# Kernel optimization log

Measured on AMD Instinct MI355X. Metric: run time of the kernel, lower is better.

The kernel has to match this reference:

```python
import jax, jax.numpy as jnp
import numpy as np

V, C, T, E, H, L = 25, 8, 14, 64, 128, 32
B = 65536


def setup_inputs() -> dict:
    key = jax.random.key(0)
    ks = jax.random.split(key, 24)
    rn = lambda k, s: jax.random.normal(k, s, dtype=jnp.float32) * 0.05
    return {
        "x": jax.random.randint(ks[0], (B, T), 0, V),
        "c": jax.random.normal(ks[1], (B, C), dtype=jnp.float32),
        "eps": jax.random.normal(ks[2], (B, L), dtype=jnp.float32),
        # encoder params
        "emb_enc": rn(ks[3], (V, E)),
        "W_ih_e": rn(ks[4], (3 * H, E)),
        "W_hh_e": rn(ks[5], (3 * H, H)),
        "b_ih_e": rn(ks[6], (3 * H,)),
        "b_hh_e": rn(ks[7], (3 * H,)),
        "W_mu": rn(ks[8], (L, H + C)),
        "b_mu": rn(ks[9], (L,)),
        "W_lv": rn(ks[10], (L, H + C)),
        "b_lv": rn(ks[11], (L,)),
        # decoder params
        "emb_dec": rn(ks[12], (V, E)),
        "W_fch": rn(ks[13], (H, L + C)),
        "b_fch": rn(ks[14], (H,)),
        "W_ih_d": rn(ks[15], (3 * H, E + L + C)),
        "W_hh_d": rn(ks[16], (3 * H, H)),
        "b_ih_d": rn(ks[17], (3 * H,)),
        "b_hh_d": rn(ks[18], (3 * H,)),
        "W_out": rn(ks[19], (V, H)),
        "b_out": rn(ks[20], (V,)),
    }


def gru_seq(x_proj, h0, W_hh, b_hh):
    """PyTorch-style GRU. x_proj: [B,T,3H] = input @ W_ih.T + b_ih (precomputed)."""
    def step(h, xp):
        gh = h @ W_hh.T + b_hh
        i_r, i_z, i_n = jnp.split(xp, 3, axis=-1)
        h_r, h_z, h_n = jnp.split(gh, 3, axis=-1)
        r = jax.nn.sigmoid(i_r + h_r)
        zg = jax.nn.sigmoid(i_z + h_z)
        n = jnp.tanh(i_n + r * h_n)
        h_new = (1.0 - zg) * n + zg * h
        return h_new, h_new
    hT, hs = jax.lax.scan(step, h0, jnp.swapaxes(x_proj, 0, 1))
    return hT, hs  # hs: [T,B,H]


def reference(x, c, eps, emb_enc, W_ih_e, W_hh_e, b_ih_e, b_hh_e, W_mu, b_mu,
              W_lv, b_lv, emb_dec, W_fch, b_fch, W_ih_d, W_hh_d, b_ih_d,
              b_hh_d, W_out, b_out):
    Bn = x.shape[0]
    Hn = W_hh_e.shape[1]
    # ---- encoder ----
    emb = emb_enc[x]                                   # [B,T,E]
    xp = emb @ W_ih_e.T + b_ih_e                       # [B,T,3H]
    h_enc, _ = gru_seq(xp, jnp.zeros((Bn, Hn), emb.dtype), W_hh_e, b_hh_e)
    hc = jnp.concatenate([h_enc, c], axis=1)           # [B,H+C]
    mu = hc @ W_mu.T + b_mu
    logvar = hc @ W_lv.T + b_lv
    # ---- reparameterize ----
    z = mu + eps * jnp.exp(0.5 * logvar)
    # ---- decoder (teacher forced on x[:, :-1]) ----
    context = jnp.concatenate([z, c], axis=1)          # [B,L+C]
    h0 = context @ W_fch.T + b_fch                     # [B,H]
    dec_in = x[:, :-1]                                 # [B,T-1]
    emb_d = emb_dec[dec_in]                            # [B,T-1,E]
    Tm1 = dec_in.shape[1]
    ctx_b = jnp.broadcast_to(context[:, None, :], (Bn, Tm1, context.shape[1]))
    step_in = jnp.concatenate([emb_d, ctx_b], axis=-1)  # [B,T-1,E+L+C]
    xp_d = step_in @ W_ih_d.T + b_ih_d                 # [B,T-1,3H]
    _, hs = gru_seq(xp_d, h0, W_hh_d, b_hh_d)          # [T-1,B,H]
    recon = jnp.einsum('tbh,vh->btv', hs, W_out) + b_out  # [B,T-1,V]
    return recon, mu, logvar
```

## Files before the change

### kernel.cpp

```cpp
#include <hip/hip_runtime.h>

typedef __bf16 bf16x8 __attribute__((ext_vector_type(8)));
typedef __bf16 bf16x4 __attribute__((ext_vector_type(4)));
typedef float  floatx4 __attribute__((ext_vector_type(4)));

#define Vv 25
#define Tt 14
#define Ee 64
#define Hh 128
#define Ll 32
#define Ccc 8
#define G3 384
#define TABP 388
#define HP   136
#define CXP  72

#define MFMA16(a, b, c) __builtin_amdgcn_mfma_f32_16x16x32_bf16(a, b, c, 0, 0, 0)

extern "C" __global__ void __launch_bounds__(256)
cvae_tables(const float* __restrict__ emb_enc, const float* __restrict__ W_ih_e,
            const float* __restrict__ b_ih_e, const float* __restrict__ b_hh_e,
            const float* __restrict__ emb_dec, const float* __restrict__ W_ih_d,
            float* __restrict__ ws)
{
    int id = blockIdx.x * 256 + threadIdx.x;
    if (id >= 2 * Vv * G3) return;
    int half = id / (Vv * G3);
    int r = id % (Vv * G3);
    int v = r / G3, j = r % G3;
    if (half == 0) {
        float acc = b_ih_e[j] + (j < 2 * Hh ? b_hh_e[j] : 0.0f);
        const float* e = emb_enc + v * Ee;
        const float* wp = W_ih_e + j * Ee;
        #pragma unroll 4
        for (int k = 0; k < Ee; k++) acc += e[k] * wp[k];
        ws[v * G3 + j] = acc;
    } else {
        float acc = 0.0f;
        const float* e = emb_dec + v * Ee;
        const float* wp = W_ih_d + j * 104;
        #pragma unroll 4
        for (int k = 0; k < Ee; k++) acc += e[k] * wp[k];
        ws[Vv * G3 + v * G3 + j] = acc;
    }
}

__device__ __forceinline__ float rcp_f(float x) { return __builtin_amdgcn_rcpf(x); }
__device__ __forceinline__ float sigm(float x)  { return rcp_f(1.0f + __expf(-x)); }
__device__ __forceinline__ float tanhg(float x) { return 1.0f - 2.0f * rcp_f(1.0f + __expf(2.0f * x)); }

extern "C" __global__ void __launch_bounds__(512, 2)
cvae_mfma(const int* __restrict__ x, const float* __restrict__ cin,
          const float* __restrict__ eps,
          const float* __restrict__ W_hh_e, const float* __restrict__ b_hh_e,
          const float* __restrict__ W_mu, const float* __restrict__ b_mu,
          const float* __restrict__ W_lv, const float* __restrict__ b_lv,
          const float* __restrict__ W_fch, const float* __restrict__ b_fch,
          const float* __restrict__ W_ih_d, const float* __restrict__ W_hh_d,
          const float* __restrict__ b_ih_d, const float* __restrict__ b_hh_d,
          const float* __restrict__ W_out, const float* __restrict__ b_out,
          const float* __restrict__ tabs, float* __restrict__ out, int Btot)
{
    __shared__ __align__(16) __bf16 hA[64 * HP];
    __shared__ __align__(16) __bf16 hB[64 * HP];
    __shared__ __align__(16) __bf16 tab_s[Vv * TABP];
    __shared__ __align__(16) __bf16 ctx_s[64 * CXP];
    __shared__ unsigned char x_s[64 * Tt];

    const int tid  = threadIdx.x;
    const int w    = tid >> 6;
    const int lane = tid & 63;
    const int li   = lane & 15;
    const int q    = lane >> 4;
    const int b0   = blockIdx.x * 64;
    const size_t MU_OFF = (size_t)Btot * 13 * Vv;
    const size_t LV_OFF = MU_OFF + (size_t)Btot * Ll;
    const floatx4 zf = {0.f, 0.f, 0.f, 0.f};

    for (int i = tid; i < 64 * Tt; i += 512)
        x_s[i] = (unsigned char)x[(size_t)b0 * Tt + i];
    for (int i = tid; i < Vv * G3; i += 512)
        tab_s[(i / G3) * TABP + (i % G3)] = (__bf16)tabs[i];
    {
        int b = tid >> 3, cc = tid & 7;
        ctx_s[b * CXP + Ll + cc] = (__bf16)cin[((size_t)b0 + b) * Ccc + cc];
        #pragma unroll
        for (int k3 = 0; k3 < 3; k3++) {
            int i = tid * 3 + k3;
            ctx_s[(i / 24) * CXP + 40 + (i % 24)] = (__bf16)0.f;
        }
    }

    bf16x8 aW[3][4];
    #pragma unroll
    for (int role = 0; role < 3; role++)
        #pragma unroll
        for (int kb = 0; kb < 4; kb++) {
            const float* p = W_hh_e + (role * Hh + w * 16 + li) * Hh + kb * 32 + q * 8;
            bf16x8 f;
            #pragma unroll
            for (int jj = 0; jj < 8; jj++) f[jj] = (__bf16)p[jj];
            aW[role][kb] = f;
        }
    float bhh2[4];
    #pragma unroll
    for (int r = 0; r < 4; r++) bhh2[r] = b_hh_e[2 * Hh + w * 16 + q * 4 + r];

    float hreg[4][4];
    #pragma unroll
    for (int nt = 0; nt < 4; nt++)
        #pragma unroll
        for (int r = 0; r < 4; r++) hreg[nt][r] = 0.f;

    __syncthreads();

    for (int t = 0; t < Tt; t++) {
        const __bf16* rd = (t & 1) ? hB : hA;
        __bf16*       wr = (t & 1) ? hA : hB;

        floatx4 acc[3][4];
        if (t == 0) {
            #pragma unroll
            for (int role = 0; role < 3; role++)
                #pragma unroll
                for (int nt = 0; nt < 4; nt++) acc[role][nt] = zf;
        } else {
            bf16x8 hf[4][4];
            #pragma unroll
            for (int nt = 0; nt < 4; nt++)
                #pragma unroll
                for (int kb = 0; kb < 4; kb++)
                    hf[nt][kb] = *(const bf16x8*)&rd[(nt * 16 + li) * HP + kb * 32 + q * 8];
            #pragma unroll
            for (int role = 0; role < 3; role++)
                #pragma unroll
                for (int nt = 0; nt < 4; nt++) acc[role][nt] = zf;
            #pragma unroll
            for (int kb = 0; kb < 4; kb++)
                #pragma unroll
                for (int role = 0; role < 3; role++)
                    #pragma unroll
                    for (int nt = 0; nt < 4; nt++)
                        acc[role][nt] = MFMA16(aW[role][kb], hf[nt][kb], acc[role][nt]);
        }

        #pragma unroll
        for (int nt = 0; nt < 4; nt++) {
            int bl = nt * 16 + li;
            int tok = x_s[bl * Tt + t];
            const __bf16* tp = &tab_s[tok * TABP + w * 16 + q * 4];
            bf16x4 tR = *(const bf16x4*)(tp);
            bf16x4 tZ = *(const bf16x4*)(tp + Hh);
            bf16x4 tN = *(const bf16x4*)(tp + 2 * Hh);
            bf16x4 hv;
            #pragma unroll
            for (int r = 0; r < 4; r++) {
                float rr = sigm(acc[0][nt][r] + (float)tR[r]);
                float zz = sigm(acc[1][nt][r] + (float)tZ[r]);
                float nn = tanhg((float)tN[r] + rr * (acc[2][nt][r] + bhh2[r]));
                float h  = nn + zz * (hreg[nt][r] - nn);
                hreg[nt][r] = h;
                hv[r] = (__bf16)h;
            }
            *(bf16x4*)&wr[bl * HP + w * 16 + q * 4] = hv;
        }
        __syncthreads();
    }

    {
        for (int i = tid; i < Vv * G3; i += 512)
            tab_s[(i / G3) * TABP + (i % G3)] = (__bf16)tabs[Vv * G3 + i];

        const int mt = w & 3;
        const int lp = mt * 8 + (li >> 1);
        const float* Wsrc = (li & 1) ? W_lv : W_mu;
        bf16x8 aM[5], aE[5];
        #pragma unroll
        for (int kb = 0; kb < 5; kb++) {
            bf16x8 f = {}, f2 = {};
            if (kb < 4 || q == 0) {
                const float* p = Wsrc + lp * 136 + (kb < 4 ? kb * 32 + q * 8 : 128);
                #pragma unroll
                for (int jj = 0; jj < 8; jj++) {
                    float v = p[jj];
                    __bf16 hi = (__bf16)v;
                    f[jj]  = hi;
                    f2[jj] = (__bf16)(v - (float)hi);
                }
            }
            aM[kb] = f; aE[kb] = f2;
        }
        #pragma unroll
        for (int jn = 0; jn < 2; jn++) {
            const int nt = (w >> 2) * 2 + jn;
            floatx4 acc = zf;
            #pragma unroll
            for (int kb = 0; kb < 4; kb++) {
                bf16x8 hf = *(const bf16x8*)&hA[(nt * 16 + li) * HP + kb * 32 + q * 8];
                acc = MFMA16(aM[kb], hf, acc);
                acc = MFMA16(aE[kb], hf, acc);
            }
            {
                bf16x8 cf = {};
                if (q == 0) cf = *(const bf16x8*)&ctx_s[(nt * 16 + li) * CXP + Ll];
                acc = MFMA16(aM[4], cf, acc);
                acc = MFMA16(aE[4], cf, acc);
            }
            const int b = nt * 16 + li;
            const size_t bg = (size_t)b0 + b;
            const int l0 = mt * 8 + q * 2;
            float mu0 = acc[0] + b_mu[l0],     lv0 = acc[1] + b_lv[l0];
            float mu1 = acc[2] + b_mu[l0 + 1], lv1 = acc[3] + b_lv[l0 + 1];
            float2 ev = *(const float2*)&eps[bg * Ll + l0];
            float z0 = mu0 + ev.x * __expf(0.5f * lv0);
            float z1 = mu1 + ev.y * __expf(0.5f * lv1);
            ctx_s[b * CXP + l0]     = (__bf16)z0;
            ctx_s[b * CXP + l0 + 1] = (__bf16)z1;
            *(float2*)&out[MU_OFF + bg * Ll + l0] = make_float2(mu0, mu1);
            *(float2*)&out[LV_OFF + bg * Ll + l0] = make_float2(lv0, lv1);
        }
    }
    __syncthreads();

    floatx4 h0a[4] = {zf, zf, zf, zf};
    floatx4 base[3][4];
    #pragma unroll
    for (int role = 0; role < 3; role++)
        #pragma unroll
        for (int nt = 0; nt < 4; nt++) base[role][nt] = zf;
    #pragma unroll
    for (int kb2 = 0; kb2 < 2; kb2++) {
        bf16x8 afh, aC0, aC1, aC2;
        #pragma unroll
        for (int jj = 0; jj < 8; jj++) {
            int k = kb2 * 32 + q * 8 + jj;
            bool ok = (k < 40);
            afh[jj] = ok ? (__bf16)W_fch[(w * 16 + li) * 40 + k]                   : (__bf16)0.f;
            aC0[jj] = ok ? (__bf16)W_ih_d[(0 * Hh + w * 16 + li) * 104 + Ee + k]   : (__bf16)0.f;
            aC1[jj] = ok ? (__bf16)W_ih_d[(1 * Hh + w * 16 + li) * 104 + Ee + k]   : (__bf16)0.f;
            aC2[jj] = ok ? (__bf16)W_ih_d[(2 * Hh + w * 16 + li) * 104 + Ee + k]   : (__bf16)0.f;
        }
        #pragma unroll
        for (int nt = 0; nt < 4; nt++) {
            bf16x8 cf = *(const bf16x8*)&ctx_s[(nt * 16 + li) * CXP + kb2 * 32 + q * 8];
            h0a[nt]     = MFMA16(afh, cf, h0a[nt]);
            base[0][nt] = MFMA16(aC0, cf, base[0][nt]);
            base[1][nt] = MFMA16(aC1, cf, base[1][nt]);
            base[2][nt] = MFMA16(aC2, cf, base[2][nt]);
        }
    }
    #pragma unroll
    for (int nt = 0; nt < 4; nt++) {
        bf16x4 hv;
        #pragma unroll
        for (int r = 0; r < 4; r++) {
            float s = h0a[nt][r] + b_fch[w * 16 + q * 4 + r];
            hreg[nt][r] = s;
            hv[r] = (__bf16)s;
        }
        *(bf16x4*)&hA[(nt * 16 + li) * HP + w * 16 + q * 4] = hv;
    }
    float bhn[4];
    #pragma unroll
    for (int r = 0; r < 4; r++) {
        int j = w * 16 + q * 4 + r;
        float br = b_ih_d[j] + b_hh_d[j];
        float bz = b_ih_d[Hh + j] + b_hh_d[Hh + j];
        float bi = b_ih_d[2 * Hh + j];
        #pragma unroll
        for (int nt = 0; nt < 4; nt++) {
            base[0][nt][r] += br;
            base[1][nt][r] += bz;
            base[2][nt][r] += bi;
        }
        bhn[r] = b_hh_d[2 * Hh + j];
    }
    #pragma unroll
    for (int role = 0; role < 3; role++)
        #pragma unroll
        for (int kb = 0; kb < 4; kb++) {
            const float* p = W_hh_d + (role * Hh + w * 16 + li) * Hh + kb * 32 + q * 8;
            bf16x8 f;
            #pragma unroll
            for (int jj = 0; jj < 8; jj++) f[jj] = (__bf16)p[jj];
            aW[role][kb] = f;
        }
    const int mt_o = w & 1, nt_o = w >> 1;
    bf16x8 aO[4];
    #pragma unroll
    for (int kb = 0; kb < 4; kb++) {
        int row = mt_o * 16 + li;
        bf16x8 f;
        #pragma unroll
        for (int jj = 0; jj < 8; jj++)
            f[jj] = (row < Vv) ? (__bf16)W_out[row * Hh + kb * 32 + q * 8 + jj] : (__bf16)0.f;
        aO[kb] = f;
    }
    float bo[4];
    #pragma unroll
    for (int r = 0; r < 4; r++) {
        int v = mt_o * 16 + q * 4 + r;
        bo[r] = (v < Vv) ? b_out[v] : 0.f;
    }

    __syncthreads();

    for (int t = 0; t < Tt - 1; t++) {
        const __bf16* rdb = (t & 1) ? hB : hA;
        __bf16*       wrb = (t & 1) ? hA : hB;

        bf16x8 hf[4][4];
        #pragma unroll
        for (int nt = 0; nt < 4; nt++)
            #pragma unroll
            for (int kb = 0; kb < 4; kb++)
                hf[nt][kb] = *(const bf16x8*)&rdb[(nt * 16 + li) * HP + kb * 32 + q * 8];

        floatx4 acc[3][4];
        #pragma unroll
        for (int nt = 0; nt < 4; nt++) {
            acc[0][nt] = base[0][nt];
            acc[1][nt] = base[1][nt];
            acc[2][nt] = zf;
        }
        #pragma unroll
        for (int kb = 0; kb < 4; kb++)
            #pragma unroll
            for (int role = 0; role < 3; role++)
                #pragma unroll
                for (int nt = 0; nt < 4; nt++)
                    acc[role][nt] = MFMA16(aW[role][kb], hf[nt][kb], acc[role][nt]);

        #pragma unroll
        for (int nt = 0; nt < 4; nt++) {
            int bl = nt * 16 + li;
            int tok = x_s[bl * Tt + t];
            const __bf16* tp = &tab_s[tok * TABP + w * 16 + q * 4];
            bf16x4 tR = *(const bf16x4*)(tp);
            bf16x4 tZ = *(const bf16x4*)(tp + Hh);
            bf16x4 tN = *(const bf16x4*)(tp + 2 * Hh);
            bf16x4 hv;
            #pragma unroll
            for (int r = 0; r < 4; r++) {
                float rr = sigm(acc[0][nt][r] + (float)tR[r]);
                float zz = sigm(acc[1][nt][r] + (float)tZ[r]);
                float nn = tanhg(base[2][nt][r] + (float)tN[r] + rr * (acc[2][nt][r] + bhn[r]));
                float h  = nn + zz * (hreg[nt][r] - nn);
                hreg[nt][r] = h;
                hv[r] = (__bf16)h;
            }
            *(bf16x4*)&wrb[bl * HP + w * 16 + q * 4] = hv;
        }
        __syncthreads();

        bf16x8 of[4];
        #pragma unroll
        for (int kb = 0; kb < 4; kb++)
            of[kb] = *(const bf16x8*)&wrb[(nt_o * 16 + li) * HP + kb * 32 + q * 8];
        floatx4 po = zf;
        #pragma unroll
        for (int kb = 0; kb < 4; kb++)
            po = MFMA16(aO[kb], of[kb], po);
        #pragma unroll
        for (int r = 0; r < 4; r++) {
            int v = mt_o * 16 + q * 4 + r;
            if (v < Vv)
                out[((size_t)(b0 + nt_o * 16 + li) * 13 + t) * Vv + v] = po[r] + bo[r];
        }
    }
}

extern "C" void kernel_launch(void* const* d_in, const int* in_sizes, int n_in,
                              void* d_out, int out_size, void* d_ws, size_t ws_size,
                              hipStream_t stream)
{
    const int*   x       = (const int*)d_in[0];
    const float* c       = (const float*)d_in[1];
    const float* eps     = (const float*)d_in[2];
    const float* emb_enc = (const float*)d_in[3];
    const float* W_ih_e  = (const float*)d_in[4];
    const float* W_hh_e  = (const float*)d_in[5];
    const float* b_ih_e  = (const float*)d_in[6];
    const float* b_hh_e  = (const float*)d_in[7];
    const float* W_mu    = (const float*)d_in[8];
    const float* b_mu    = (const float*)d_in[9];
    const float* W_lv    = (const float*)d_in[10];
    const float* b_lv    = (const float*)d_in[11];
    const float* emb_dec = (const float*)d_in[12];
    const float* W_fch   = (const float*)d_in[13];
    const float* b_fch   = (const float*)d_in[14];
    const float* W_ih_d  = (const float*)d_in[15];
    const float* W_hh_d  = (const float*)d_in[16];
    const float* b_ih_d  = (const float*)d_in[17];
    const float* b_hh_d  = (const float*)d_in[18];
    const float* W_out   = (const float*)d_in[19];
    const float* b_out   = (const float*)d_in[20];

    float* ws = (float*)d_ws;
    const int Btot = in_sizes[0] / Tt;

    cvae_tables<<<75, 256, 0, stream>>>(emb_enc, W_ih_e, b_ih_e, b_hh_e, emb_dec, W_ih_d, ws);

    cvae_mfma<<<Btot / 64, 512, 0, stream>>>(
        x, c, eps, W_hh_e, b_hh_e, W_mu, b_mu, W_lv, b_lv,
        W_fch, b_fch, W_ih_d, W_hh_d, b_ih_d, b_hh_d, W_out, b_out,
        ws, (float*)d_out, Btot);
}
```

Measured before the change: 568.2 us.

## Replace LDS token table gathers with one-hot MFMA and raise occupancy

Drops the shared-memory copy of the per-token input projection tables and computes each gate's input contribution with an extra MFMA per gate, multiplying a register-resident slice of the table by a one-hot vector built from the token id. This removes roughly 19 KB of LDS and the scattered bf16x4 table reads on each step, and launch bounds are raised from 2 to 4 blocks per SM. The cost is 12 extra MFMAs per step, register pressure from holding the table slices, and a risk of spilling under the tighter register cap.

```diff
diff --git a/kernel.cpp b/kernel.cpp
--- a/kernel.cpp
+++ b/kernel.cpp
@@ -3,6 +3,7 @@
 typedef __bf16 bf16x8 __attribute__((ext_vector_type(8)));
 typedef __bf16 bf16x4 __attribute__((ext_vector_type(4)));
 typedef float  floatx4 __attribute__((ext_vector_type(4)));
+typedef unsigned int u32x4 __attribute__((ext_vector_type(4)));
 
 #define Vv 25
 #define Tt 14
@@ -11,7 +12,6 @@
 #define Ll 32
 #define Ccc 8
 #define G3 384
-#define TABP 388
 #define HP   136
 #define CXP  72
 
@@ -49,7 +49,20 @@
 __device__ __forceinline__ float sigm(float x)  { return rcp_f(1.0f + __expf(-x)); }
 __device__ __forceinline__ float tanhg(float x) { return 1.0f - 2.0f * rcp_f(1.0f + __expf(2.0f * x)); }
 
-extern "C" __global__ void __launch_bounds__(512, 2)
+__device__ __forceinline__ bf16x8 onehot8(int tok, int q)
+{
+    int u = tok - q * 8;
+    unsigned val = (u & 1) ? 0x3F800000u : 0x00003F80u;
+    int uw = u >> 1;
+    u32x4 wds;
+    wds[0] = (uw == 0) ? val : 0u;
+    wds[1] = (uw == 1) ? val : 0u;
+    wds[2] = (uw == 2) ? val : 0u;
+    wds[3] = (uw == 3) ? val : 0u;
+    return __builtin_bit_cast(bf16x8, wds);
+}
+
+extern "C" __global__ void __launch_bounds__(512, 4)
 cvae_mfma(const int* __restrict__ x, const float* __restrict__ cin,
           const float* __restrict__ eps,
           const float* __restrict__ W_hh_e, const float* __restrict__ b_hh_e,
@@ -63,7 +76,6 @@
 {
     __shared__ __align__(16) __bf16 hA[64 * HP];
     __shared__ __align__(16) __bf16 hB[64 * HP];
-    __shared__ __align__(16) __bf16 tab_s[Vv * TABP];
     __shared__ __align__(16) __bf16 ctx_s[64 * CXP];
     __shared__ unsigned char x_s[64 * Tt];
 
@@ -79,8 +91,6 @@
 
     for (int i = tid; i < 64 * Tt; i += 512)
         x_s[i] = (unsigned char)x[(size_t)b0 * Tt + i];
-    for (int i = tid; i < Vv * G3; i += 512)
-        tab_s[(i / G3) * TABP + (i % G3)] = (__bf16)tabs[i];
     {
         int b = tid >> 3, cc = tid & 7;
         ctx_s[b * CXP + Ll + cc] = (__bf16)cin[((size_t)b0 + b) * Ccc + cc];
@@ -102,6 +112,17 @@
             for (int jj = 0; jj < 8; jj++) f[jj] = (__bf16)p[jj];
             aW[role][kb] = f;
         }
+    bf16x8 aT[3];
+    #pragma unroll
+    for (int role = 0; role < 3; role++) {
+        bf16x8 f = {};
+        #pragma unroll
+        for (int jj = 0; jj < 8; jj++) {
+            int v = q * 8 + jj;
+            if (v < Vv) f[jj] = (__bf16)tabs[v * G3 + role * Hh + w * 16 + li];
+        }
+        aT[role] = f;
+    }
     float bhh2[4];
     #pragma unroll
     for (int r = 0; r < 4; r++) bhh2[r] = b_hh_e[2 * Hh + w * 16 + q * 4 + r];
@@ -118,23 +139,26 @@
         const __bf16* rd = (t & 1) ? hB : hA;
         __bf16*       wr = (t & 1) ? hA : hB;
 
-        floatx4 acc[3][4];
-        if (t == 0) {
-            #pragma unroll
-            for (int role = 0; role < 3; role++)
-                #pragma unroll
-                for (int nt = 0; nt < 4; nt++) acc[role][nt] = zf;
-        } else {
+        floatx4 acc[3][4], acc3[4];
+        #pragma unroll
+        for (int nt = 0; nt < 4; nt++) {
+            acc[0][nt] = zf; acc[1][nt] = zf; acc[2][nt] = zf; acc3[nt] = zf;
+        }
+        #pragma unroll
+        for (int nt = 0; nt < 4; nt++) {
+            int tok = x_s[(nt * 16 + li) * Tt + t];
+            bf16x8 oh = onehot8(tok, q);
+            acc[0][nt] = MFMA16(aT[0], oh, acc[0][nt]);
+            acc[1][nt] = MFMA16(aT[1], oh, acc[1][nt]);
+            acc3[nt]   = MFMA16(aT[2], oh, acc3[nt]);
+        }
+        if (t != 0) {
             bf16x8 hf[4][4];
             #pragma unroll
             for (int nt = 0; nt < 4; nt++)
                 #pragma unroll
                 for (int kb = 0; kb < 4; kb++)
                     hf[nt][kb] = *(const bf16x8*)&rd[(nt * 16 + li) * HP + kb * 32 + q * 8];
-            #pragma unroll
-            for (int role = 0; role < 3; role++)
-                #pragma unroll
-                for (int nt = 0; nt < 4; nt++) acc[role][nt] = zf;
             #pragma unroll
             for (int kb = 0; kb < 4; kb++)
                 #pragma unroll
@@ -147,17 +171,12 @@
         #pragma unroll
         for (int nt = 0; nt < 4; nt++) {
             int bl = nt * 16 + li;
-            int tok = x_s[bl * Tt + t];
-            const __bf16* tp = &tab_s[tok * TABP + w * 16 + q * 4];
-            bf16x4 tR = *(const bf16x4*)(tp);
-            bf16x4 tZ = *(const bf16x4*)(tp + Hh);
-            bf16x4 tN = *(const bf16x4*)(tp + 2 * Hh);
             bf16x4 hv;
             #pragma unroll
             for (int r = 0; r < 4; r++) {
-                float rr = sigm(acc[0][nt][r] + (float)tR[r]);
-                float zz = sigm(acc[1][nt][r] + (float)tZ[r]);
-                float nn = tanhg((float)tN[r] + rr * (acc[2][nt][r] + bhh2[r]));
+                float rr = sigm(acc[0][nt][r]);
+                float zz = sigm(acc[1][nt][r]);
+                float nn = tanhg(acc3[nt][r] + rr * (acc[2][nt][r] + bhh2[r]));
                 float h  = nn + zz * (hreg[nt][r] - nn);
                 hreg[nt][r] = h;
                 hv[r] = (__bf16)h;
@@ -168,9 +187,6 @@
     }
 
     {
-        for (int i = tid; i < Vv * G3; i += 512)
-            tab_s[(i / G3) * TABP + (i % G3)] = (__bf16)tabs[Vv * G3 + i];
-
         const int mt = w & 3;
         const int lp = mt * 8 + (li >> 1);
         const float* Wsrc = (li & 1) ? W_lv : W_mu;
@@ -285,6 +301,16 @@
             for (int jj = 0; jj < 8; jj++) f[jj] = (__bf16)p[jj];
             aW[role][kb] = f;
         }
+    #pragma unroll
+    for (int role = 0; role < 3; role++) {
+        bf16x8 f = {};
+        #pragma unroll
+        for (int jj = 0; jj < 8; jj++) {
+            int v = q * 8 + jj;
+            if (v < Vv) f[jj] = (__bf16)tabs[Vv * G3 + v * G3 + role * Hh + w * 16 + li];
+        }
+        aT[role] = f;
+    }
     const int mt_o = w & 1, nt_o = w >> 1;
     bf16x8 aO[4];
     #pragma unroll
@@ -309,20 +335,29 @@
         const __bf16* rdb = (t & 1) ? hB : hA;
         __bf16*       wrb = (t & 1) ? hA : hB;
 
-        bf16x8 hf[4][4];
-        #pragma unroll
-        for (int nt = 0; nt < 4; nt++)
-            #pragma unroll
-            for (int kb = 0; kb < 4; kb++)
-                hf[nt][kb] = *(const bf16x8*)&rdb[(nt * 16 + li) * HP + kb * 32 + q * 8];
-
-        floatx4 acc[3][4];
+        floatx4 acc[3][4], acc3[4];
         #pragma unroll
         for (int nt = 0; nt < 4; nt++) {
             acc[0][nt] = base[0][nt];
             acc[1][nt] = base[1][nt];
             acc[2][nt] = zf;
-        }
+            acc3[nt]   = zf;
+        }
+        #pragma unroll
+        for (int nt = 0; nt < 4; nt++) {
+            int tok = x_s[(nt * 16 + li) * Tt + t];
+            bf16x8 oh = onehot8(tok, q);
+            acc[0][nt] = MFMA16(aT[0], oh, acc[0][nt]);
+            acc[1][nt] = MFMA16(aT[1], oh, acc[1][nt]);
+            acc3[nt]   = MFMA16(aT[2], oh, acc3[nt]);
+        }
+
+        bf16x8 hf[4][4];
+        #pragma unroll
+        for (int nt = 0; nt < 4; nt++)
+            #pragma unroll
+            for (int kb = 0; kb < 4; kb++)
+                hf[nt][kb] = *(const bf16x8*)&rdb[(nt * 16 + li) * HP + kb * 32 + q * 8];
         #pragma unroll
         for (int kb = 0; kb < 4; kb++)
             #pragma unroll
@@ -334,17 +369,12 @@
         #pragma unroll
         for (int nt = 0; nt < 4; nt++) {
             int bl = nt * 16 + li;
-            int tok = x_s[bl * Tt + t];
-            const __bf16* tp = &tab_s[tok * TABP + w * 16 + q * 4];
-            bf16x4 tR = *(const bf16x4*)(tp);
-            bf16x4 tZ = *(const bf16x4*)(tp + Hh);
-            bf16x4 tN = *(const bf16x4*)(tp + 2 * Hh);
             bf16x4 hv;
             #pragma unroll
             for (int r = 0; r < 4; r++) {
-                float rr = sigm(acc[0][nt][r] + (float)tR[r]);
-                float zz = sigm(acc[1][nt][r] + (float)tZ[r]);
-                float nn = tanhg(base[2][nt][r] + (float)tN[r] + rr * (acc[2][nt][r] + bhn[r]));
+                float rr = sigm(acc[0][nt][r]);
+                float zz = sigm(acc[1][nt][r]);
+                float nn = tanhg(base[2][nt][r] + acc3[nt][r] + rr * (acc[2][nt][r] + bhn[r]));
                 float h  = nn + zz * (hreg[nt][r] - nn);
                 hreg[nt][r] = h;
                 hv[r] = (__bf16)h;
```

New measurement: 1.157 ms. 2.04x slower.

## Fuse embedding-projection table build into main kernel via split-bf16 MFMA

Applied to the files above, without the earlier changes.

Removes the separate table-precompute kernel and has each block compute the encoder and decoder embedding×W_ih tables in-kernel with MFMA, using a hi/lo bf16 split to keep near-fp32 accuracy. This drops one kernel launch and the global workspace round-trip. In exchange every one of the 1024 blocks redoes the small table GEMM, which adds per-block prologue work and register pressure. It also folds the hidden-bias of the n gate into the MFMA accumulator initialisation instead of adding it in the gate math.

```diff
diff --git a/kernel.cpp b/kernel.cpp
--- a/kernel.cpp
+++ b/kernel.cpp
@@ -17,34 +17,6 @@
 
 #define MFMA16(a, b, c) __builtin_amdgcn_mfma_f32_16x16x32_bf16(a, b, c, 0, 0, 0)
 
-extern "C" __global__ void __launch_bounds__(256)
-cvae_tables(const float* __restrict__ emb_enc, const float* __restrict__ W_ih_e,
-            const float* __restrict__ b_ih_e, const float* __restrict__ b_hh_e,
-            const float* __restrict__ emb_dec, const float* __restrict__ W_ih_d,
-            float* __restrict__ ws)
-{
-    int id = blockIdx.x * 256 + threadIdx.x;
-    if (id >= 2 * Vv * G3) return;
-    int half = id / (Vv * G3);
-    int r = id % (Vv * G3);
-    int v = r / G3, j = r % G3;
-    if (half == 0) {
-        float acc = b_ih_e[j] + (j < 2 * Hh ? b_hh_e[j] : 0.0f);
-        const float* e = emb_enc + v * Ee;
-        const float* wp = W_ih_e + j * Ee;
-        #pragma unroll 4
-        for (int k = 0; k < Ee; k++) acc += e[k] * wp[k];
-        ws[v * G3 + j] = acc;
-    } else {
-        float acc = 0.0f;
-        const float* e = emb_dec + v * Ee;
-        const float* wp = W_ih_d + j * 104;
-        #pragma unroll 4
-        for (int k = 0; k < Ee; k++) acc += e[k] * wp[k];
-        ws[Vv * G3 + v * G3 + j] = acc;
-    }
-}
-
 __device__ __forceinline__ float rcp_f(float x) { return __builtin_amdgcn_rcpf(x); }
 __device__ __forceinline__ float sigm(float x)  { return rcp_f(1.0f + __expf(-x)); }
 __device__ __forceinline__ float tanhg(float x) { return 1.0f - 2.0f * rcp_f(1.0f + __expf(2.0f * x)); }
@@ -52,14 +24,17 @@
 extern "C" __global__ void __launch_bounds__(512, 2)
 cvae_mfma(const int* __restrict__ x, const float* __restrict__ cin,
           const float* __restrict__ eps,
+          const float* __restrict__ emb_enc, const float* __restrict__ W_ih_e,
+          const float* __restrict__ b_ih_e,
           const float* __restrict__ W_hh_e, const float* __restrict__ b_hh_e,
           const float* __restrict__ W_mu, const float* __restrict__ b_mu,
           const float* __restrict__ W_lv, const float* __restrict__ b_lv,
+          const float* __restrict__ emb_dec,
           const float* __restrict__ W_fch, const float* __restrict__ b_fch,
           const float* __restrict__ W_ih_d, const float* __restrict__ W_hh_d,
           const float* __restrict__ b_ih_d, const float* __restrict__ b_hh_d,
           const float* __restrict__ W_out, const float* __restrict__ b_out,
-          const float* __restrict__ tabs, float* __restrict__ out, int Btot)
+          float* __restrict__ out, int Btot)
 {
     __shared__ __align__(16) __bf16 hA[64 * HP];
     __shared__ __align__(16) __bf16 hB[64 * HP];
@@ -79,8 +54,6 @@
 
     for (int i = tid; i < 64 * Tt; i += 512)
         x_s[i] = (unsigned char)x[(size_t)b0 * Tt + i];
-    for (int i = tid; i < Vv * G3; i += 512)
-        tab_s[(i / G3) * TABP + (i % G3)] = (__bf16)tabs[i];
     {
         int b = tid >> 3, cc = tid & 7;
         ctx_s[b * CXP + Ll + cc] = (__bf16)cin[((size_t)b0 + b) * Ccc + cc];
@@ -91,6 +64,58 @@
         }
     }
 
+    #pragma unroll
+    for (int role = 0; role < 3; role++) {
+        const int j0 = role * Hh + w * 16;
+        bf16x8 aH[2], aR[2];
+        #pragma unroll
+        for (int kb2 = 0; kb2 < 2; kb2++) {
+            const float* p = W_ih_e + (j0 + li) * Ee + kb2 * 32 + q * 8;
+            #pragma unroll
+            for (int jj = 0; jj < 8; jj++) {
+                float v = p[jj]; __bf16 hi = (__bf16)v;
+                aH[kb2][jj] = hi; aR[kb2][jj] = (__bf16)(v - (float)hi);
+            }
+        }
+        floatx4 c[2] = {zf, zf};
+        #pragma unroll
+        for (int ntb = 0; ntb < 2; ntb++) {
+            int v = ntb * 16 + li;
+            bf16x8 bH[2], bR[2];
+            #pragma unroll
+            for (int kb2 = 0; kb2 < 2; kb2++) {
+                #pragma unroll
+                for (int jj = 0; jj < 8; jj++) {
+                    float e = (v < Vv) ? emb_enc[v * Ee + kb2 * 32 + q * 8 + jj] : 0.f;
+                    __bf16 hi = (__bf16)e;
+                    bH[kb2][jj] = hi; bR[kb2][jj] = (__bf16)(e - (float)hi);
+                }
+            }
+            #pragma unroll
+            for (int kb2 = 0; kb2 < 2; kb2++) {
+                c[ntb] = MFMA16(aH[kb2], bH[kb2], c[ntb]);
+                c[ntb] = MFMA16(aR[kb2], bH[kb2], c[ntb]);
+                c[ntb] = MFMA16(aH[kb2], bR[kb2], c[ntb]);
+            }
+        }
+        float bb[4];
+        #pragma unroll
+        for (int r = 0; r < 4; r++) {
+            int j = j0 + q * 4 + r;
+            bb[r] = b_ih_e[j] + (role < 2 ? b_hh_e[j] : 0.f);
+        }
+        #pragma unroll
+        for (int ntb = 0; ntb < 2; ntb++) {
+            int v = ntb * 16 + li;
+            if (v < Vv) {
+                bf16x4 tv;
+                #pragma unroll
+                for (int r = 0; r < 4; r++) tv[r] = (__bf16)(c[ntb][r] + bb[r]);
+                *(bf16x4*)&tab_s[v * TABP + j0 + q * 4] = tv;
+            }
+        }
+    }
+
     bf16x8 aW[3][4];
     #pragma unroll
     for (int role = 0; role < 3; role++)
@@ -102,9 +127,9 @@
             for (int jj = 0; jj < 8; jj++) f[jj] = (__bf16)p[jj];
             aW[role][kb] = f;
         }
-    float bhh2[4];
-    #pragma unroll
-    for (int r = 0; r < 4; r++) bhh2[r] = b_hh_e[2 * Hh + w * 16 + q * 4 + r];
+    floatx4 bh2v;
+    #pragma unroll
+    for (int r = 0; r < 4; r++) bh2v[r] = b_hh_e[2 * Hh + w * 16 + q * 4 + r];
 
     float hreg[4][4];
     #pragma unroll
@@ -119,22 +144,17 @@
         __bf16*       wr = (t & 1) ? hA : hB;
 
         floatx4 acc[3][4];
-        if (t == 0) {
-            #pragma unroll
-            for (int role = 0; role < 3; role++)
-                #pragma unroll
-                for (int nt = 0; nt < 4; nt++) acc[role][nt] = zf;
-        } else {
+        #pragma unroll
+        for (int nt = 0; nt < 4; nt++) {
+            acc[0][nt] = zf; acc[1][nt] = zf; acc[2][nt] = bh2v;
+        }
+        if (t != 0) {
             bf16x8 hf[4][4];
             #pragma unroll
             for (int nt = 0; nt < 4; nt++)
                 #pragma unroll
                 for (int kb = 0; kb < 4; kb++)
                     hf[nt][kb] = *(const bf16x8*)&rd[(nt * 16 + li) * HP + kb * 32 + q * 8];
-            #pragma unroll
-            for (int role = 0; role < 3; role++)
-                #pragma unroll
-                for (int nt = 0; nt < 4; nt++) acc[role][nt] = zf;
             #pragma unroll
             for (int kb = 0; kb < 4; kb++)
                 #pragma unroll
@@ -157,7 +177,7 @@
             for (int r = 0; r < 4; r++) {
                 float rr = sigm(acc[0][nt][r] + (float)tR[r]);
                 float zz = sigm(acc[1][nt][r] + (float)tZ[r]);
-                float nn = tanhg((float)tN[r] + rr * (acc[2][nt][r] + bhh2[r]));
+                float nn = tanhg((float)tN[r] + rr * acc[2][nt][r]);
                 float h  = nn + zz * (hreg[nt][r] - nn);
                 hreg[nt][r] = h;
                 hv[r] = (__bf16)h;
@@ -168,8 +188,51 @@
     }
 
     {
-        for (int i = tid; i < Vv * G3; i += 512)
-            tab_s[(i / G3) * TABP + (i % G3)] = (__bf16)tabs[Vv * G3 + i];
+        #pragma unroll
+        for (int role = 0; role < 3; role++) {
+            const int j0 = role * Hh + w * 16;
+            bf16x8 aH[2], aR[2];
+            #pragma unroll
+            for (int kb2 = 0; kb2 < 2; kb2++) {
+                const float* p = W_ih_d + (j0 + li) * 104 + kb2 * 32 + q * 8;
+                #pragma unroll
+                for (int jj = 0; jj < 8; jj++) {
+                    float v = p[jj]; __bf16 hi = (__bf16)v;
+                    aH[kb2][jj] = hi; aR[kb2][jj] = (__bf16)(v - (float)hi);
+                }
+            }
+            floatx4 c[2] = {zf, zf};
+            #pragma unroll
+            for (int ntb = 0; ntb < 2; ntb++) {
+                int v = ntb * 16 + li;
+                bf16x8 bH[2], bR[2];
+                #pragma unroll
+                for (int kb2 = 0; kb2 < 2; kb2++) {
+                    #pragma unroll
+                    for (int jj = 0; jj < 8; jj++) {
+                        float e = (v < Vv) ? emb_dec[v * Ee + kb2 * 32 + q * 8 + jj] : 0.f;
+                        __bf16 hi = (__bf16)e;
+                        bH[kb2][jj] = hi; bR[kb2][jj] = (__bf16)(e - (float)hi);
+                    }
+                }
+                #pragma unroll
+                for (int kb2 = 0; kb2 < 2; kb2++) {
+                    c[ntb] = MFMA16(aH[kb2], bH[kb2], c[ntb]);
+                    c[ntb] = MFMA16(aR[kb2], bH[kb2], c[ntb]);
+                    c[ntb] = MFMA16(aH[kb2], bR[kb2], c[ntb]);
+                }
+            }
+            #pragma unroll
+            for (int ntb = 0; ntb < 2; ntb++) {
+                int v = ntb * 16 + li;
+                if (v < Vv) {
+                    bf16x4 tv;
+                    #pragma unroll
+                    for (int r = 0; r < 4; r++) tv[r] = (__bf16)c[ntb][r];
+                    *(bf16x4*)&tab_s[v * TABP + j0 + q * 4] = tv;
+                }
+            }
+        }
 
         const int mt = w & 3;
         const int lp = mt * 8 + (li >> 1);
@@ -260,7 +323,7 @@
         }
         *(bf16x4*)&hA[(nt * 16 + li) * HP + w * 16 + q * 4] = hv;
     }
-    float bhn[4];
+    floatx4 bhnv;
     #pragma unroll
     for (int r = 0; r < 4; r++) {
         int j = w * 16 + q * 4 + r;
@@ -273,7 +336,7 @@
             base[1][nt][r] += bz;
             base[2][nt][r] += bi;
         }
-        bhn[r] = b_hh_d[2 * Hh + j];
+        bhnv[r] = b_hh_d[2 * Hh + j];
     }
     #pragma unroll
     for (int role = 0; role < 3; role++)
@@ -309,20 +372,20 @@
         const __bf16* rdb = (t & 1) ? hB : hA;
         __bf16*       wrb = (t & 1) ? hA : hB;
 
+        floatx4 acc[3][4];
+        #pragma unroll
+        for (int nt = 0; nt < 4; nt++) {
+            acc[0][nt] = base[0][nt];
+            acc[1][nt] = base[1][nt];
+            acc[2][nt] = bhnv;
+        }
+
         bf16x8 hf[4][4];
         #pragma unroll
         for (int nt = 0; nt < 4; nt++)
             #pragma unroll
             for (int kb = 0; kb < 4; kb++)
                 hf[nt][kb] = *(const bf16x8*)&rdb[(nt * 16 + li) * HP + kb * 32 + q * 8];
-
-        floatx4 acc[3][4];
-        #pragma unroll
-        for (int nt = 0; nt < 4; nt++) {
-            acc[0][nt] = base[0][nt];
-            acc[1][nt] = base[1][nt];
-            acc[2][nt] = zf;
-        }
         #pragma unroll
         for (int kb = 0; kb < 4; kb++)
             #pragma unroll
@@ -344,7 +407,7 @@
             for (int r = 0; r < 4; r++) {
                 float rr = sigm(acc[0][nt][r] + (float)tR[r]);
                 float zz = sigm(acc[1][nt][r] + (float)tZ[r]);
-                float nn = tanhg(base[2][nt][r] + (float)tN[r] + rr * (acc[2][nt][r] + bhn[r]));
+                float nn = tanhg(base[2][nt][r] + (float)tN[r] + rr * acc[2][nt][r]);
                 float h  = nn + zz * (hreg[nt][r] - nn);
                 hreg[nt][r] = h;
                 hv[r] = (__bf16)h;
@@ -396,13 +459,11 @@
     const float* W_out   = (const float*)d_in[19];
     const float* b_out   = (const float*)d_in[20];
 
-    float* ws = (float*)d_ws;
     const int Btot = in_sizes[0] / Tt;
 
-    cvae_tables<<<75, 256, 0, stream>>>(emb_enc, W_ih_e, b_ih_e, b_hh_e, emb_dec, W_ih_d, ws);
-
     cvae_mfma<<<Btot / 64, 512, 0, stream>>>(
-        x, c, eps, W_hh_e, b_hh_e, W_mu, b_mu, W_lv, b_lv,
-        W_fch, b_fch, W_ih_d, W_hh_d, b_ih_d, b_hh_d, W_out, b_out,
-        ws, (float*)d_out, Btot);
+        x, c, eps, emb_enc, W_ih_e, b_ih_e, W_hh_e, b_hh_e,
+        W_mu, b_mu, W_lv, b_lv, emb_dec, W_fch, b_fch,
+        W_ih_d, W_hh_d, b_ih_d, b_hh_d, W_out, b_out,
+        (float*)d_out, Btot);
 }
```

After: 602.2 us. +6.0%, slower.
